# Kernel tuning notes

Hardware: AMD Instinct MI355X
Metric: run time of the kernel (lower is better)

## Reference

```python
import jax, jax.numpy as jnp
import numpy as np

B, S, HID = 2, 2048, 2048
H, HK, D = 32, 8, 64
N_REP = H // HK
SCALE = D ** -0.5


def setup_inputs() -> dict:
    key = jax.random.key(0)
    ks = jax.random.split(key, 9)
    std = HID ** -0.5
    causal = jnp.tril(jnp.ones((S, S), dtype=bool))
    attention_mask = jnp.where(causal, 0.0, -1e9).astype(jnp.float32)[None, None]  # [1,1,S,S]
    return {
        "hidden_states": jax.random.normal(ks[0], (B, S, HID), jnp.float32),
        "attention_mask": attention_mask,
        "q_w": jax.random.normal(ks[1], (HID, H * D), jnp.float32) * std,
        "q_b": jax.random.normal(ks[2], (H * D,), jnp.float32) * 0.01,
        "k_w": jax.random.normal(ks[3], (HID, HK * D), jnp.float32) * std,
        "k_b": jax.random.normal(ks[4], (HK * D,), jnp.float32) * 0.01,
        "v_w": jax.random.normal(ks[5], (HID, HK * D), jnp.float32) * std,
        "v_b": jax.random.normal(ks[6], (HK * D,), jnp.float32) * 0.01,
        "dense_w": jax.random.normal(ks[7], (HID, HID), jnp.float32) * std,
        "dense_b": jax.random.normal(ks[8], (HID,), jnp.float32) * 0.01,
    }


def reference(hidden_states, attention_mask, q_w, q_b, k_w, k_b, v_w, v_b, dense_w, dense_b):
    b, s, _ = hidden_states.shape
    # projections -> [b, h, s, d]
    q = (hidden_states @ q_w + q_b).reshape(b, s, H, D).transpose(0, 2, 1, 3)
    k = (hidden_states @ k_w + k_b).reshape(b, s, HK, D).transpose(0, 2, 1, 3)
    v = (hidden_states @ v_w + v_b).reshape(b, s, HK, D).transpose(0, 2, 1, 3)
    # GQA: repeat_kv (repeat_interleave along head dim)
    k = jnp.repeat(k, N_REP, axis=1)  # [b, H, s, d]
    v = jnp.repeat(v, N_REP, axis=1)
    # eager attention: full score matrix
    scores = jnp.einsum("bhqd,bhkd->bhqk", q, k) * SCALE + attention_mask
    w = jax.nn.softmax(scores.astype(jnp.float32), axis=-1).astype(q.dtype)
    attn = jnp.einsum("bhqk,bhkd->bhqd", w, v)
    attn = attn.transpose(0, 2, 1, 3).reshape(b, s, H * D)
    return attn @ dense_w + dense_b
```

## Files before the change

### kernel.cpp

```cpp
#include <hip/hip_runtime.h>
#include <hip/hip_bf16.h>


typedef short s16x8 __attribute__((ext_vector_type(8)));
typedef float f32x4 __attribute__((ext_vector_type(4)));

static constexpr int BB = 2, SS = 2048, HID = 2048, HH = 32, HKV = 8, DD = 64;
static constexpr int MM = BB * SS;
static constexpr int NQKV = 3072;

#define DEV __device__ __forceinline__

DEV short f2bf(float f) {
    unsigned u = __builtin_bit_cast(unsigned, f);
    return (short)((u + 0x7fffu + ((u >> 16) & 1u)) >> 16);
}

DEV unsigned cvtpk(float lo, float hi) {
    unsigned r;
    asm("v_cvt_pk_bf16_f32 %0, %1, %2" : "=v"(r) : "v"(lo), "v"(hi));
    return r;
}

DEV void stage16(const short* gsrc, short* lbase) {
    __builtin_amdgcn_global_load_lds((const __attribute__((address_space(1))) void*)gsrc,
                                     (__attribute__((address_space(3))) void*)lbase, 16, 0, 0);
}

__global__ __launch_bounds__(256) void cvt_f32_bf16(const float* __restrict__ in,
                                                    short* __restrict__ out, int n) {
    int i = (blockIdx.x * 256 + threadIdx.x) * 8;
    if (i >= n) return;
    float4 a = *reinterpret_cast<const float4*>(in + i);
    float4 b = *reinterpret_cast<const float4*>(in + i + 4);
    s16x8 o;
    o[0] = f2bf(a.x); o[1] = f2bf(a.y); o[2] = f2bf(a.z); o[3] = f2bf(a.w);
    o[4] = f2bf(b.x); o[5] = f2bf(b.y); o[6] = f2bf(b.z); o[7] = f2bf(b.w);
    *reinterpret_cast<s16x8*>(out + i) = o;
}

__global__ __launch_bounds__(256) void transpose_cvt(const float* __restrict__ in,
                                                     short* __restrict__ out,
                                                     int K, int N) {
    __shared__ float tile[32][33];
    int k0 = blockIdx.x * 32, n0 = blockIdx.y * 32;
    int tx = threadIdx.x & 31, ty = threadIdx.x >> 5;
#pragma unroll
    for (int r = ty; r < 32; r += 8)
        tile[r][tx] = in[(size_t)(k0 + r) * N + n0 + tx];
    __syncthreads();
#pragma unroll
    for (int r = ty; r < 32; r += 8)
        out[(size_t)(n0 + r) * K + k0 + tx] = f2bf(tile[tx][r]);
}

__global__ __launch_bounds__(256) void transpose_v(const short* __restrict__ QKV,
                                                   short* __restrict__ Vtg) {
    __shared__ int tile[32][33];
    const int s0 = blockIdx.x * 32, c0 = blockIdx.y * 32, b = blockIdx.z;
    const int tx = threadIdx.x & 31, ty = threadIdx.x >> 5;
#pragma unroll
    for (int r = ty; r < 32; r += 8)
        tile[r][tx] = QKV[(size_t)(b * SS + s0 + r) * NQKV + 2560 + c0 + tx];
    __syncthreads();
#pragma unroll
    for (int r = ty; r < 32; r += 8) {
        const int c = c0 + r;
        Vtg[((size_t)(b * HKV + (c >> 6)) * 64 + (c & 63)) * SS + s0 + tx] = (short)tile[tx][r];
    }
}

__global__ __launch_bounds__(256) void concat_bias(const float* __restrict__ qb,
                                                   const float* __restrict__ kb,
                                                   const float* __restrict__ vb,
                                                   float* __restrict__ cb) {
    int i = blockIdx.x * 256 + threadIdx.x;
    if (i < 2048) cb[i] = qb[i];
    else if (i < 2560) cb[i] = kb[i - 2048];
    else if (i < 3072) cb[i] = vb[i - 2560];
}

template <int BM, int BN, typename OutT>
__global__ __launch_bounds__(512) void gemm8p(const short* __restrict__ A,
                                              const short* __restrict__ Bt,
                                              const float* __restrict__ bias,
                                              OutT* __restrict__ C,
                                              int M, int N, int K, int qcols) {
    constexpr int NR = BN / 64;
    constexpr int ACH = BM * 4;
    constexpr int BCH = BN * 4;
    static_assert(ACH % 512 == 0, "A chunks per half must be thread-uniform");
    constexpr int SA = ACH / 512;
    __shared__ __align__(16) short lds[(BM + BN) * 128];
    const int tid = threadIdx.x, lane = tid & 63, wid = tid >> 6;
    const int fr = lane & 15, fk = lane >> 4;
    const int wm = wid >> 2, wn = wid & 3;
    const int nbn = N / BN;
    const int cpx = gridDim.x >> 3;
    const int wg = (blockIdx.x & 7) * cpx + (blockIdx.x >> 3);
    const int bm = wg / nbn, bn = wg % nbn;
    const int NT = K / 64;

    const short* Ablk = A + (size_t)bm * BM * K;
    const short* Bblk = Bt + (size_t)bn * BN * K;

    auto abase = [&](int bf, int kh) { return bf * (BM * 64) + kh * (BM * 32); };
    auto bbase = [&](int bf, int kh) { return 2 * (BM * 64) + bf * (BN * 64) + kh * (BN * 32); };

    auto stA = [&](int bf, int kh, int kt) {
#pragma unroll
        for (int l = 0; l < SA; ++l) {
            const int c = l * 512 + tid;
            const int r = c >> 2, sg = (c & 3) ^ ((r >> 1) & 3);
            stage16(Ablk + (size_t)r * K + kt + kh * 32 + sg * 8,
                    &lds[abase(bf, kh) + (l * 512 + wid * 64) * 8]);
        }
    };
    auto stB = [&](int bf, int kh, int kt) {
        {
            const int c = tid;
            const int r = c >> 2, sg = (c & 3) ^ ((r >> 1) & 3);
            stage16(Bblk + (size_t)r * K + kt + kh * 32 + sg * 8,
                    &lds[bbase(bf, kh) + (wid * 64) * 8]);
        }
        if constexpr (BCH > 512) {
            if (tid < BCH - 512) {
                const int c = 512 + tid;
                const int r = c >> 2, sg = (c & 3) ^ ((r >> 1) & 3);
                stage16(Bblk + (size_t)r * K + kt + kh * 32 + sg * 8,
                        &lds[bbase(bf, kh) + ((512 + wid * 64)) * 8]);
            }
        }
    };

    auto waithalf = [&](bool pf) {
        if (!pf) { asm volatile("s_waitcnt vmcnt(0)" ::: "memory"); return; }
        if constexpr (BCH > 512) {
            if (wid < (BCH - 512) / 64) asm volatile("s_waitcnt vmcnt(4)" ::: "memory");
            else                        asm volatile("s_waitcnt vmcnt(3)" ::: "memory");
        } else {
            asm volatile("s_waitcnt vmcnt(3)" ::: "memory");
        }
    };

    f32x4 acc[8][NR] = {};

    stA(0, 0, 0); stB(0, 0, 0);
    stA(0, 1, 0); stB(0, 1, 0);
    waithalf(true);
    asm volatile("s_barrier" ::: "memory");

    for (int t = 0; t < NT; ++t) {
        const int bf = t & 1, sf = bf ^ 1;
        const int ktn = (t + 1) * 64;
        const bool pf = (t + 1 < NT);
#pragma unroll
        for (int kh = 0; kh < 2; ++kh) {
            s16x8 bfrag[NR], afrag[8];
#pragma unroll
            for (int n = 0; n < NR; ++n) {
                const int row = wn * (BN / 4) + n * 16 + fr;
                bfrag[n] = *reinterpret_cast<const s16x8*>(
                    &lds[bbase(bf, kh) + row * 32 + ((fk ^ ((row >> 1) & 3)) * 8)]);
            }
#pragma unroll
            for (int i = 0; i < 8; ++i) {
                const int row = wm * 128 + i * 16 + fr;
                afrag[i] = *reinterpret_cast<const s16x8*>(
                    &lds[abase(bf, kh) + row * 32 + ((fk ^ ((row >> 1) & 3)) * 8)]);
            }
            if (pf) stA(sf, kh, ktn);
            __builtin_amdgcn_s_setprio(1);
#pragma unroll
            for (int i = 0; i < 4; ++i)
#pragma unroll
                for (int n = 0; n < NR; ++n)
                    acc[i][n] = __builtin_amdgcn_mfma_f32_16x16x32_bf16(
                        afrag[i], bfrag[n], acc[i][n], 0, 0, 0);
            __builtin_amdgcn_s_setprio(0);
            if (pf) stB(sf, kh, ktn);
            __builtin_amdgcn_s_setprio(1);
#pragma unroll
            for (int i = 4; i < 8; ++i)
#pragma unroll
                for (int n = 0; n < NR; ++n)
                    acc[i][n] = __builtin_amdgcn_mfma_f32_16x16x32_bf16(
                        afrag[i], bfrag[n], acc[i][n], 0, 0, 0);
            __builtin_amdgcn_s_setprio(0);
            waithalf(pf);
            asm volatile("s_barrier" ::: "memory");
        }
    }

#pragma unroll
    for (int n = 0; n < NR; ++n) {
        const int col = bn * BN + wn * (BN / 4) + n * 16 + fr;
        const float bv = bias[col];
        const float sc = (col < qcols) ? 0.125f : 1.0f;
#pragma unroll
        for (int mi = 0; mi < 8; ++mi) {
            const int row0 = bm * BM + wm * 128 + mi * 16 + fk * 4;
#pragma unroll
            for (int r = 0; r < 4; ++r) {
                const float v = (acc[mi][n][r] + bv) * sc;
                if constexpr (sizeof(OutT) == 2)
                    reinterpret_cast<short*>(C)[(size_t)(row0 + r) * N + col] = f2bf(v);
                else
                    reinterpret_cast<float*>(C)[(size_t)(row0 + r) * N + col] = v;
            }
        }
    }
}

__global__ __launch_bounds__(256, 2) void attn_fwd(
        const short* __restrict__ QKV,
        const short* __restrict__ Vtg,
        short* __restrict__ Ob) {
    constexpr int KB = 64;
    __shared__ __align__(16) short Qs[128 * 64];
    __shared__ __align__(16) short Ks[2][KB * 64];
    __shared__ __align__(16) short Vt[2][64 * 64];
    __shared__ __align__(16) short Ps[128 * 64];

    const int pair = blockIdx.x;
    const int bh = blockIdx.y;
    const int b = bh >> 5, h = bh & 31;
    const int kvh = h >> 2;
    const int tid = threadIdx.x, lane = tid & 63, wid = tid >> 6;
    const int fr = lane & 15, fk = lane >> 4;
    const int wq0 = wid * 32;

    const short* kbase = QKV + (size_t)b * SS * NQKV + 2048 + kvh * DD;
    const short* vbase = Vtg + (size_t)(b * HKV + kvh) * 64 * SS;

    auto stageKV = [&](int bb, int kv0) {
#pragma unroll
        for (int is = 0; is < 2; ++is) {
            const int c = is * 256 + wid * 64 + lane;
            const int r = c >> 3, sg = (c & 7) ^ (r & 7);
            stage16(kbase + (size_t)(kv0 + r) * NQKV + sg * 8,
                    &Ks[bb][(is * 256 + wid * 64) * 8]);
            stage16(vbase + (size_t)r * SS + kv0 + sg * 8,
                    &Vt[bb][(is * 256 + wid * 64) * 8]);
        }
    };
    auto stageQ = [&](int q0) {
        const short* qbase = QKV + ((size_t)b * SS + q0) * NQKV + h * DD;
#pragma unroll
        for (int is = 0; is < 4; ++is) {
            const int c = is * 256 + wid * 64 + lane;
            const int r = c >> 3, sg = (c & 7) ^ (r & 7);
            stage16(qbase + (size_t)r * NQKV + sg * 8,
                    &Qs[(is * 256 + wid * 64) * 8]);
        }
    };

    s16x8 ones = {};
    if (fr == 0) {
#pragma unroll
        for (int e = 0; e < 8; ++e) ones[e] = (short)0x3F80;
    }

    int cur = 0;
    stageQ(pair * 128);
    stageKV(0, 0);

    for (int sidx = 0; sidx < 2; ++sidx) {
        const int strip = sidx ? (15 - pair) : pair;
        const int q0 = strip * 128;
        const size_t qrow0 = (size_t)b * SS + q0;
        const int nt = 2 * strip + 2;

        __syncthreads();

        s16x8 bq[2][2];
#pragma unroll
        for (int i = 0; i < 2; ++i)
#pragma unroll
            for (int ks = 0; ks < 2; ++ks) {
                const int row = wq0 + i * 16 + fr;
                const int byte = (ks * 64 + fk * 16) ^ ((row & 7) << 4);
                bq[i][ks] = *reinterpret_cast<const s16x8*>(
                    reinterpret_cast<const char*>(Qs) + row * 128 + byte);
            }

        f32x4 acc_o[2][4] = {};
        f32x4 acc_l[2] = {};

        for (int t = 0; t < nt; ++t) {
            const int kv0 = t * KB;
            if (t + 1 < nt) {
                stageKV(cur ^ 1, kv0 + KB);
            } else if (sidx == 0) {
                stageQ((15 - pair) * 128);
                stageKV(cur ^ 1, 0);
            }

            f32x4 sacc[2][4] = {};
            __builtin_amdgcn_s_setprio(1);
#pragma unroll
            for (int j = 0; j < 4; ++j)
#pragma unroll
                for (int ks = 0; ks < 2; ++ks) {
                    const int row = j * 16 + fr;
                    const int byte = (ks * 64 + fk * 16) ^ ((row & 7) << 4);
                    s16x8 kf = *reinterpret_cast<const s16x8*>(
                        reinterpret_cast<const char*>(Ks[cur]) + row * 128 + byte);
#pragma unroll
                    for (int i = 0; i < 2; ++i)
                        sacc[i][j] = __builtin_amdgcn_mfma_f32_16x16x32_bf16(kf, bq[i][ks], sacc[i][j], 0, 0, 0);
                }
            __builtin_amdgcn_s_setprio(0);

            if (kv0 + KB - 1 > q0 + wq0) {
#pragma unroll
                for (int i = 0; i < 2; ++i) {
                    const int qg = q0 + wq0 + i * 16 + fr;
#pragma unroll
                    for (int j = 0; j < 4; ++j) {
                        const int kvb = kv0 + j * 16 + fk * 4;
#pragma unroll
                        for (int r = 0; r < 4; ++r)
                            if (kvb + r > qg) sacc[i][j][r] = -INFINITY;
                    }
                }
            }

#pragma unroll
            for (int i = 0; i < 2; ++i) {
                char* pbase = reinterpret_cast<char*>(Ps) + (wq0 + i * 16 + fr) * 128;
#pragma unroll
                for (int j = 0; j < 4; ++j)
#pragma unroll
                    for (int hh = 0; hh < 2; ++hh) {
                        const unsigned pw = cvtpk(__expf(sacc[i][j][2 * hh]),
                                                  __expf(sacc[i][j][2 * hh + 1]));
                        const int byte = ((j * 8 + fk * 2 + hh) << 2) ^ ((fr & 7) << 4);
                        *reinterpret_cast<unsigned*>(pbase + byte) = pw;
                    }
            }

            s16x8 ap[2][2];
#pragma unroll
            for (int i = 0; i < 2; ++i) {
                const char* pbase = reinterpret_cast<const char*>(Ps) + (wq0 + i * 16 + fr) * 128;
#pragma unroll
                for (int ks = 0; ks < 2; ++ks) {
                    const int byte = ((ks * 4 + fk) * 16) ^ ((fr & 7) << 4);
                    ap[i][ks] = *reinterpret_cast<const s16x8*>(pbase + byte);
                }
            }

            __builtin_amdgcn_s_setprio(1);
#pragma unroll
            for (int jd = 0; jd < 4; ++jd)
#pragma unroll
                for (int ks = 0; ks < 2; ++ks) {
                    const int row = jd * 16 + fr;
                    const int byte = (ks * 64 + fk * 16) ^ ((row & 7) << 4);
                    s16x8 bv = *reinterpret_cast<const s16x8*>(
                        reinterpret_cast<const char*>(Vt[cur]) + row * 128 + byte);
#pragma unroll
                    for (int i = 0; i < 2; ++i)
                        acc_o[i][jd] = __builtin_amdgcn_mfma_f32_16x16x32_bf16(ap[i][ks], bv, acc_o[i][jd], 0, 0, 0);
                }
#pragma unroll
            for (int i = 0; i < 2; ++i)
#pragma unroll
                for (int ks = 0; ks < 2; ++ks)
                    acc_l[i] = __builtin_amdgcn_mfma_f32_16x16x32_bf16(ap[i][ks], ones, acc_l[i], 0, 0, 0);
            __builtin_amdgcn_s_setprio(0);

            __syncthreads();
            cur ^= 1;
        }

#pragma unroll
        for (int i = 0; i < 2; ++i)
#pragma unroll
            for (int r = 0; r < 4; ++r) {
                const float l = __shfl(acc_l[i][r], (lane & 48));
                const float inv = 1.f / l;
                const size_t grow = (qrow0 + wq0 + i * 16 + fk * 4 + r) * (size_t)(HH * DD) + h * DD;
#pragma unroll
                for (int jd = 0; jd < 4; ++jd)
                    Ob[grow + jd * 16 + fr] = f2bf(acc_o[i][jd][r] * inv);
            }
    }
}

extern "C" void kernel_launch(void* const* d_in, const int* in_sizes, int n_in,
                              void* d_out, int out_size, void* d_ws, size_t ws_size,
                              hipStream_t stream) {
    const float* hidden  = (const float*)d_in[0];
    const float* q_w     = (const float*)d_in[2];
    const float* q_b     = (const float*)d_in[3];
    const float* k_w     = (const float*)d_in[4];
    const float* k_b     = (const float*)d_in[5];
    const float* v_w     = (const float*)d_in[6];
    const float* v_b     = (const float*)d_in[7];
    const float* dense_w = (const float*)d_in[8];
    const float* dense_b = (const float*)d_in[9];
    float* out = (float*)d_out;

    short* wt   = (short*)d_ws;
    short* dwt  = wt + 6291456;
    short* QKV  = dwt + 4194304;
    short* Vtg  = QKV + 12582912;
    short* hidb = Vtg + 2097152;
    short* Ob   = hidb;
    float* cbias = (float*)(hidb + 8388608);

    cvt_f32_bf16<<<4096, 256, 0, stream>>>(hidden, hidb, MM * HID);
    transpose_cvt<<<dim3(64, 64), 256, 0, stream>>>(q_w, wt, HID, HH * DD);
    transpose_cvt<<<dim3(64, 16), 256, 0, stream>>>(k_w, wt + 2048 * 2048, HID, HKV * DD);
    transpose_cvt<<<dim3(64, 16), 256, 0, stream>>>(v_w, wt + 2560 * 2048, HID, HKV * DD);
    transpose_cvt<<<dim3(64, 64), 256, 0, stream>>>(dense_w, dwt, HID, HID);
    concat_bias<<<12, 256, 0, stream>>>(q_b, k_b, v_b, cbias);

    gemm8p<256, 192, short><<<256, 512, 0, stream>>>(hidb, wt, cbias, QKV, MM, NQKV, HID, 2048);

    transpose_v<<<dim3(64, 16, 2), 256, 0, stream>>>(QKV, Vtg);

    attn_fwd<<<dim3(8, 64), 256, 0, stream>>>(QKV, Vtg, Ob);

    gemm8p<256, 128, float><<<256, 512, 0, stream>>>(Ob, dwt, dense_b, out, MM, HID, HID, 0);
}
```

Measured before the change: 181.0 us.

## Switch GEMMs to 128x128 tiles, merge weight transposes, use exp2 softmax

Replaces the 512-thread 256xN GEMM with a 256-thread 128x128 tile kernel and launches more blocks (768 and 512), aiming for better CU occupancy and load balance on the QKV and output projections. It also merges the four weight transpose launches into two by using blockIdx.z to pick between a pair of inputs. Softmax exponentiation switches from __expf to raw v_exp_f32 (exp2), with log2(e) folded into the Q scale. Smaller tiles mean less operand reuse per block and more global traffic.

```diff
diff --git a/kernel.cpp b/kernel.cpp
--- a/kernel.cpp
+++ b/kernel.cpp
@@ -8,6 +8,7 @@
 static constexpr int BB = 2, SS = 2048, HID = 2048, HH = 32, HKV = 8, DD = 64;
 static constexpr int MM = BB * SS;
 static constexpr int NQKV = 3072;
+static constexpr float QSCALE = 0.18033688011112042f;
 
 #define DEV __device__ __forceinline__
 
@@ -19,6 +20,12 @@
 DEV unsigned cvtpk(float lo, float hi) {
     unsigned r;
     asm("v_cvt_pk_bf16_f32 %0, %1, %2" : "=v"(r) : "v"(lo), "v"(hi));
+    return r;
+}
+
+DEV float fexp2(float x) {
+    float r;
+    asm("v_exp_f32 %0, %1" : "=v"(r) : "v"(x));
     return r;
 }
 
@@ -39,10 +46,14 @@
     *reinterpret_cast<s16x8*>(out + i) = o;
 }
 
-__global__ __launch_bounds__(256) void transpose_cvt(const float* __restrict__ in,
-                                                     short* __restrict__ out,
-                                                     int K, int N) {
+__global__ __launch_bounds__(256) void transpose_cvt2(const float* __restrict__ in0,
+                                                      short* __restrict__ out0,
+                                                      const float* __restrict__ in1,
+                                                      short* __restrict__ out1,
+                                                      int K, int N) {
     __shared__ float tile[32][33];
+    const float* in = blockIdx.z ? in1 : in0;
+    short* out = blockIdx.z ? out1 : out0;
     int k0 = blockIdx.x * 32, n0 = blockIdx.y * 32;
     int tx = threadIdx.x & 31, ty = threadIdx.x >> 5;
 #pragma unroll
@@ -80,70 +91,52 @@
     else if (i < 3072) cb[i] = vb[i - 2560];
 }
 
-template <int BM, int BN, typename OutT>
-__global__ __launch_bounds__(512) void gemm8p(const short* __restrict__ A,
-                                              const short* __restrict__ Bt,
-                                              const float* __restrict__ bias,
-                                              OutT* __restrict__ C,
-                                              int M, int N, int K, int qcols) {
-    constexpr int NR = BN / 64;
-    constexpr int ACH = BM * 4;
-    constexpr int BCH = BN * 4;
-    static_assert(ACH % 512 == 0, "A chunks per half must be thread-uniform");
-    constexpr int SA = ACH / 512;
-    __shared__ __align__(16) short lds[(BM + BN) * 128];
+template <typename OutT>
+__global__ __launch_bounds__(256) void gemm128(const short* __restrict__ A,
+                                               const short* __restrict__ Bt,
+                                               const float* __restrict__ bias,
+                                               OutT* __restrict__ C,
+                                               int M, int N, int K, int qcols) {
+    __shared__ __align__(16) short lds[256 * 128];
     const int tid = threadIdx.x, lane = tid & 63, wid = tid >> 6;
     const int fr = lane & 15, fk = lane >> 4;
-    const int wm = wid >> 2, wn = wid & 3;
-    const int nbn = N / BN;
+    const int wm = wid >> 1, wn = wid & 1;
+    const int nbn = N / 128;
     const int cpx = gridDim.x >> 3;
     const int wg = (blockIdx.x & 7) * cpx + (blockIdx.x >> 3);
     const int bm = wg / nbn, bn = wg % nbn;
     const int NT = K / 64;
 
-    const short* Ablk = A + (size_t)bm * BM * K;
-    const short* Bblk = Bt + (size_t)bn * BN * K;
-
-    auto abase = [&](int bf, int kh) { return bf * (BM * 64) + kh * (BM * 32); };
-    auto bbase = [&](int bf, int kh) { return 2 * (BM * 64) + bf * (BN * 64) + kh * (BN * 32); };
+    const short* Ablk = A + (size_t)bm * 128 * K;
+    const short* Bblk = Bt + (size_t)bn * 128 * K;
+
+    auto abase = [&](int bf, int kh) { return bf * (128 * 64) + kh * (128 * 32); };
+    auto bbase = [&](int bf, int kh) { return 2 * (128 * 64) + bf * (128 * 64) + kh * (128 * 32); };
 
     auto stA = [&](int bf, int kh, int kt) {
 #pragma unroll
-        for (int l = 0; l < SA; ++l) {
-            const int c = l * 512 + tid;
+        for (int l = 0; l < 2; ++l) {
+            const int c = l * 256 + tid;
             const int r = c >> 2, sg = (c & 3) ^ ((r >> 1) & 3);
             stage16(Ablk + (size_t)r * K + kt + kh * 32 + sg * 8,
-                    &lds[abase(bf, kh) + (l * 512 + wid * 64) * 8]);
+                    &lds[abase(bf, kh) + (l * 256 + wid * 64) * 8]);
         }
     };
     auto stB = [&](int bf, int kh, int kt) {
-        {
-            const int c = tid;
+#pragma unroll
+        for (int l = 0; l < 2; ++l) {
+            const int c = l * 256 + tid;
             const int r = c >> 2, sg = (c & 3) ^ ((r >> 1) & 3);
             stage16(Bblk + (size_t)r * K + kt + kh * 32 + sg * 8,
-                    &lds[bbase(bf, kh) + (wid * 64) * 8]);
-        }
-        if constexpr (BCH > 512) {
-            if (tid < BCH - 512) {
-                const int c = 512 + tid;
-                const int r = c >> 2, sg = (c & 3) ^ ((r >> 1) & 3);
-                stage16(Bblk + (size_t)r * K + kt + kh * 32 + sg * 8,
-                        &lds[bbase(bf, kh) + ((512 + wid * 64)) * 8]);
-            }
+                    &lds[bbase(bf, kh) + (l * 256 + wid * 64) * 8]);
         }
     };
-
     auto waithalf = [&](bool pf) {
-        if (!pf) { asm volatile("s_waitcnt vmcnt(0)" ::: "memory"); return; }
-        if constexpr (BCH > 512) {
-            if (wid < (BCH - 512) / 64) asm volatile("s_waitcnt vmcnt(4)" ::: "memory");
-            else                        asm volatile("s_waitcnt vmcnt(3)" ::: "memory");
-        } else {
-            asm volatile("s_waitcnt vmcnt(3)" ::: "memory");
-        }
+        if (pf) asm volatile("s_waitcnt vmcnt(4)" ::: "memory");
+        else    asm volatile("s_waitcnt vmcnt(0)" ::: "memory");
     };
 
-    f32x4 acc[8][NR] = {};
+    f32x4 acc[4][4] = {};
 
     stA(0, 0, 0); stB(0, 0, 0);
     stA(0, 1, 0); stB(0, 1, 0);
@@ -156,34 +149,34 @@
         const bool pf = (t + 1 < NT);
 #pragma unroll
         for (int kh = 0; kh < 2; ++kh) {
-            s16x8 bfrag[NR], afrag[8];
-#pragma unroll
-            for (int n = 0; n < NR; ++n) {
-                const int row = wn * (BN / 4) + n * 16 + fr;
+            s16x8 bfrag[4], afrag[4];
+#pragma unroll
+            for (int n = 0; n < 4; ++n) {
+                const int row = wn * 64 + n * 16 + fr;
                 bfrag[n] = *reinterpret_cast<const s16x8*>(
                     &lds[bbase(bf, kh) + row * 32 + ((fk ^ ((row >> 1) & 3)) * 8)]);
             }
 #pragma unroll
-            for (int i = 0; i < 8; ++i) {
-                const int row = wm * 128 + i * 16 + fr;
+            for (int i = 0; i < 4; ++i) {
+                const int row = wm * 64 + i * 16 + fr;
                 afrag[i] = *reinterpret_cast<const s16x8*>(
                     &lds[abase(bf, kh) + row * 32 + ((fk ^ ((row >> 1) & 3)) * 8)]);
             }
             if (pf) stA(sf, kh, ktn);
             __builtin_amdgcn_s_setprio(1);
 #pragma unroll
-            for (int i = 0; i < 4; ++i)
-#pragma unroll
-                for (int n = 0; n < NR; ++n)
+            for (int i = 0; i < 2; ++i)
+#pragma unroll
+                for (int n = 0; n < 4; ++n)
                     acc[i][n] = __builtin_amdgcn_mfma_f32_16x16x32_bf16(
                         afrag[i], bfrag[n], acc[i][n], 0, 0, 0);
             __builtin_amdgcn_s_setprio(0);
             if (pf) stB(sf, kh, ktn);
             __builtin_amdgcn_s_setprio(1);
 #pragma unroll
-            for (int i = 4; i < 8; ++i)
-#pragma unroll
-                for (int n = 0; n < NR; ++n)
+            for (int i = 2; i < 4; ++i)
+#pragma unroll
+                for (int n = 0; n < 4; ++n)
                     acc[i][n] = __builtin_amdgcn_mfma_f32_16x16x32_bf16(
                         afrag[i], bfrag[n], acc[i][n], 0, 0, 0);
             __builtin_amdgcn_s_setprio(0);
@@ -193,13 +186,13 @@
     }
 
 #pragma unroll
-    for (int n = 0; n < NR; ++n) {
-        const int col = bn * BN + wn * (BN / 4) + n * 16 + fr;
+    for (int n = 0; n < 4; ++n) {
+        const int col = bn * 128 + wn * 64 + n * 16 + fr;
         const float bv = bias[col];
-        const float sc = (col < qcols) ? 0.125f : 1.0f;
-#pragma unroll
-        for (int mi = 0; mi < 8; ++mi) {
-            const int row0 = bm * BM + wm * 128 + mi * 16 + fk * 4;
+        const float sc = (col < qcols) ? QSCALE : 1.0f;
+#pragma unroll
+        for (int mi = 0; mi < 4; ++mi) {
+            const int row0 = bm * 128 + wm * 64 + mi * 16 + fk * 4;
 #pragma unroll
             for (int r = 0; r < 4; ++r) {
                 const float v = (acc[mi][n][r] + bv) * sc;
@@ -333,8 +326,8 @@
                 for (int j = 0; j < 4; ++j)
 #pragma unroll
                     for (int hh = 0; hh < 2; ++hh) {
-                        const unsigned pw = cvtpk(__expf(sacc[i][j][2 * hh]),
-                                                  __expf(sacc[i][j][2 * hh + 1]));
+                        const unsigned pw = cvtpk(fexp2(sacc[i][j][2 * hh]),
+                                                  fexp2(sacc[i][j][2 * hh + 1]));
                         const int byte = ((j * 8 + fk * 2 + hh) << 2) ^ ((fr & 7) << 4);
                         *reinterpret_cast<unsigned*>(pbase + byte) = pw;
                     }
@@ -412,17 +405,16 @@
     float* cbias = (float*)(hidb + 8388608);
 
     cvt_f32_bf16<<<4096, 256, 0, stream>>>(hidden, hidb, MM * HID);
-    transpose_cvt<<<dim3(64, 64), 256, 0, stream>>>(q_w, wt, HID, HH * DD);
-    transpose_cvt<<<dim3(64, 16), 256, 0, stream>>>(k_w, wt + 2048 * 2048, HID, HKV * DD);
-    transpose_cvt<<<dim3(64, 16), 256, 0, stream>>>(v_w, wt + 2560 * 2048, HID, HKV * DD);
-    transpose_cvt<<<dim3(64, 64), 256, 0, stream>>>(dense_w, dwt, HID, HID);
+    transpose_cvt2<<<dim3(64, 64, 2), 256, 0, stream>>>(q_w, wt, dense_w, dwt, HID, HID);
+    transpose_cvt2<<<dim3(64, 16, 2), 256, 0, stream>>>(k_w, wt + 2048 * 2048,
+                                                        v_w, wt + 2560 * 2048, HID, HKV * DD);
     concat_bias<<<12, 256, 0, stream>>>(q_b, k_b, v_b, cbias);
 
-    gemm8p<256, 192, short><<<256, 512, 0, stream>>>(hidb, wt, cbias, QKV, MM, NQKV, HID, 2048);
+    gemm128<short><<<768, 256, 0, stream>>>(hidb, wt, cbias, QKV, MM, NQKV, HID, 2048);
 
     transpose_v<<<dim3(64, 16, 2), 256, 0, stream>>>(QKV, Vtg);
 
     attn_fwd<<<dim3(8, 64), 256, 0, stream>>>(QKV, Vtg, Ob);
 
-    gemm8p<256, 128, float><<<256, 512, 0, stream>>>(Ob, dwt, dense_b, out, MM, HID, HID, 0);
-}
+    gemm128<float><<<512, 256, 0, stream>>>(Ob, dwt, dense_b, out, MM, HID, HID, 0);
+}
```

After: 181.3 us. About the same (+0.2%).
